# Kernel optimization log

Measured on AMD Instinct MI355X. Metric: run time of the kernel, lower is better.

The kernel has to match this reference:

```python
import jax, jax.numpy as jnp
import numpy as np

SCORE_THRESH = 0.25
NMS_THRESH = 0.45
DETECTIONS = 100   # self.detections
K_CAND = 300       # fixed pre-NMS candidate count (jit-friendly stand-in for torch.where filtering)
STRIDES = (8, 16, 32)


def setup_inputs() -> dict:
    key = jax.random.key(0)
    ks = jax.random.split(key, 5)
    pred_p3 = jax.random.normal(ks[0], (16, 80, 80, 3, 85), jnp.float32)
    pred_p4 = jax.random.normal(ks[1], (16, 40, 40, 3, 85), jnp.float32)
    pred_p5 = jax.random.normal(ks[2], (16, 20, 20, 3, 85), jnp.float32)
    anchors = jnp.array([[[10, 13], [16, 30], [33, 23]],
                         [[30, 61], [62, 45], [59, 119]],
                         [[116, 90], [156, 198], [373, 326]]], jnp.float32)
    image_shapes = jnp.full((16, 2), 640, jnp.int32)  # (h, w) per image
    scale_factors = jax.random.uniform(ks[3], (16,), jnp.float32, 0.5, 1.5)
    return {"pred_p3": pred_p3, "pred_p4": pred_p4, "pred_p5": pred_p5,
            "anchors": anchors, "image_shapes": image_shapes,
            "scale_factors": scale_factors, "max_size": 4096}


def _decode_level(p, stride, anchor_wh):
    # p: [B,H,W,A,5+C] already sigmoided
    B, H, W, A, _ = p.shape
    gx = jnp.arange(W, dtype=p.dtype)
    gy = jnp.arange(H, dtype=p.dtype)
    grid = jnp.stack(jnp.meshgrid(gx, gy, indexing='xy'), axis=-1)  # [H,W,2] = (x,y)
    xy = (2.0 * p[..., :2] - 0.5 + grid[None, :, :, None, :]) * stride
    wh = 4.0 * p[..., 2:4] ** 2 * anchor_wh  # anchor_wh: [A,2]
    box = jnp.concatenate([xy, wh], axis=-1).reshape(B, H * W * A, 4)
    obj = p[..., 4].reshape(B, H * W * A)
    cls = p[..., 5:].reshape(B, H * W * A, -1)
    return box, obj, cls


def _pairwise_iou(b):  # b: [K,4] xyxy
    area = (b[:, 2] - b[:, 0]) * (b[:, 3] - b[:, 1])
    lt = jnp.maximum(b[:, None, :2], b[None, :, :2])
    rb = jnp.minimum(b[:, None, 2:], b[None, :, 2:])
    wh = jnp.clip(rb - lt, 0.0)
    inter = wh[..., 0] * wh[..., 1]
    return inter / (area[:, None] + area[None, :] - inter + 1e-9)


def _nms_image(boxes, scores, labels, im_shape, scale, max_size):
    # boxes [K,4], scores [K] sorted desc, labels [K] int
    w = im_shape[1].astype(boxes.dtype)
    h = im_shape[0].astype(boxes.dtype)
    boxes = jnp.stack([jnp.clip(boxes[:, 0], 0.0, w), jnp.clip(boxes[:, 1], 0.0, h),
                       jnp.clip(boxes[:, 2], 0.0, w), jnp.clip(boxes[:, 3], 0.0, h)], axis=1)
    # class-offset boxes (batched_nms)
    bn = jax.lax.stop_gradient(boxes + (labels.astype(boxes.dtype) * max_size)[:, None])
    iou = _pairwise_iou(bn)
    s_ng = jax.lax.stop_gradient(scores)
    K = boxes.shape[0]
    ar = jnp.arange(K)

    def body(i, keep):
        active = keep[i] & (s_ng[i] > SCORE_THRESH)
        return keep & ~((iou[i] > NMS_THRESH) & (ar > i) & active)

    keep = jax.lax.fori_loop(0, K, body, jnp.ones(K, bool))
    final = jnp.where(keep & (s_ng > SCORE_THRESH), scores, 0.0)
    det_s, det_i = jax.lax.top_k(final, DETECTIONS)
    det_b = boxes[det_i] / scale
    det_l = labels[det_i].astype(boxes.dtype)
    return jnp.concatenate([det_b, det_s[:, None], det_l[:, None]], axis=1)  # [D,6]


def reference(pred_p3, pred_p4, pred_p5, anchors, image_shapes, scale_factors, max_size):
    boxes_l, obj_l, cls_l = [], [], []
    for i, (pred, stride) in enumerate(zip((pred_p3, pred_p4, pred_p5), STRIDES)):
        p = jax.nn.sigmoid(pred)
        b, o, c = _decode_level(p, float(stride), anchors[i])
        boxes_l.append(b); obj_l.append(o); cls_l.append(c)
    boxes = jnp.concatenate(boxes_l, axis=1)   # [B,N,4] cxcywh
    obj = jnp.concatenate(obj_l, axis=1)       # [B,N]
    cls = jnp.concatenate(cls_l, axis=1)       # [B,N,C]
    # cxcywh -> xyxy
    cx, cy, ww, hh = boxes[..., 0], boxes[..., 1], boxes[..., 2], boxes[..., 3]
    boxes = jnp.stack([cx - ww / 2, cy - hh / 2, cx + ww / 2, cy + hh / 2], axis=-1)
    B, N, C = cls.shape
    logits = obj[..., None] * cls              # [B,N,C]
    valid = (obj[..., None] > SCORE_THRESH) & (logits > SCORE_THRESH)
    flat = jnp.where(valid, logits, 0.0).reshape(B, N * C)
    vals, idx = jax.lax.top_k(flat, K_CAND)    # sorted desc per image
    aidx = idx // C
    labels = idx % C
    cand_boxes = jnp.take_along_axis(boxes, aidx[..., None], axis=1)  # [B,K,4]
    out = jax.vmap(_nms_image, in_axes=(0, 0, 0, 0, 0, None))(
        cand_boxes, vals, labels, image_shapes, scale_factors, jnp.float32(max_size))
    return out  # [B, DETECTIONS, 6] = (x1,y1,x2,y2,score,label)
```

## Files before the change

kernel.cpp:

```cpp
#include <hip/hip_runtime.h>
#include <cstdint>
#include <cstddef>

#define BATCH 16
#define NCLS 80
#define NANCH 25200
#define G 48
#define NCHUNK 525
#define TOTCH (BATCH * NCHUNK)
#define CPB 4
#define ABINS 512
#define SBINS 1024
#define ACAP 2048
#define SCAP 2048
#define TILE 64
#define KC 300
#define DET 100
#define SCORE_T 0.25f
#define NMS_T 0.45f

__device__ __forceinline__ float sg(float x) { return 1.0f / (1.0f + expf(-x)); }

__device__ __forceinline__ const float* anchor_base(const float* p3, const float* p4,
                                                    const float* p5, int b, int n) {
    if (n < 19200) return p3 + ((size_t)b * 19200 + n) * 85;
    if (n < 24000) return p4 + ((size_t)b * 4800 + (n - 19200)) * 85;
    return p5 + ((size_t)b * 1200 + (n - 24000)) * 85;
}

struct Chunk { const float4* p; int outbase; };
__device__ __forceinline__ Chunk chunk_of(int g, const float* p3, const float* p4,
                                          const float* p5) {
    Chunk ck;
    int b = g / NCHUNK, ch = g % NCHUNK;
    const float* src; int a0, lvlN, gbase;
    if (ch < 400)      { src = p3; a0 = ch * G;         lvlN = 19200; gbase = 0; }
    else if (ch < 500) { src = p4; a0 = (ch - 400) * G; lvlN = 4800;  gbase = 19200; }
    else               { src = p5; a0 = (ch - 500) * G; lvlN = 1200;  gbase = 24000; }
    ck.p = (const float4*)(src + ((size_t)b * lvlN + a0) * 85);
    ck.outbase = b * NANCH + gbase + a0;
    return ck;
}

__global__ __launch_bounds__(256) void k_max(const float* __restrict__ p3,
                                             const float* __restrict__ p4,
                                             const float* __restrict__ p5,
                                             float* __restrict__ gmax) {
    __shared__ __align__(16) float buf[G * 85];
    __shared__ float pmax[5 * G];
    int tid = threadIdx.x;
    int g0 = blockIdx.x * CPB;
    Chunk cur = chunk_of(g0, p3, p4, p5);
    float4 pre[4];
#pragma unroll
    for (int r = 0; r < 4; r++) {
        int i = tid + r * 256;
        pre[r] = (i < (G * 85 / 4)) ? cur.p[i] : make_float4(0.f, 0.f, 0.f, 0.f);
    }
    for (int it = 0; it < CPB; ++it) {
#pragma unroll
        for (int r = 0; r < 4; r++) {
            int i = tid + r * 256;
            if (i < (G * 85 / 4)) ((float4*)buf)[i] = pre[r];
        }
        Chunk nxt = cur;
        if (it + 1 < CPB) {
            nxt = chunk_of(g0 + it + 1, p3, p4, p5);
#pragma unroll
            for (int r = 0; r < 4; r++) {
                int i = tid + r * 256;
                pre[r] = (i < (G * 85 / 4)) ? nxt.p[i] : make_float4(0.f, 0.f, 0.f, 0.f);
            }
        }
        __syncthreads();
        if (tid < 240) {
            int a = tid % G, part = tid / G;
            const float* base = buf + a * 85 + 5 + part * 16;
            float m = base[0];
#pragma unroll
            for (int k = 1; k < 16; k++) m = fmaxf(m, base[k]);
            pmax[part * G + a] = m;
        }
        __syncthreads();
        if (tid < G) {
            float m = pmax[tid];
#pragma unroll
            for (int p = 1; p < 5; p++) m = fmaxf(m, pmax[p * G + tid]);
            float obj = sg(buf[tid * 85 + 4]);
            float v = 0.0f;
            if (obj > SCORE_T) v = obj * sg(m);
            gmax[cur.outbase + tid] = v;
        }
        __syncthreads();
        cur = nxt;
    }
}

union Ovl {
    struct { float tile[TILE * 85]; } p1;
    struct {
        unsigned long long msk[KC * 5];
        float4 bx[KC];
        int lab[KC];
        float sc2[KC];
        float ar[KC];
        unsigned long long keep[5];
        unsigned int actw[10];
        int wpref[6];
        int order[DET];
        int okept[DET];
    } p2;
};

__global__ __launch_bounds__(1024) void k_img(
    const float* __restrict__ p3, const float* __restrict__ p4, const float* __restrict__ p5,
    const float* __restrict__ anchors, const int* __restrict__ imshapes,
    const float* __restrict__ scalef, const float* __restrict__ gmax,
    float* __restrict__ out) {
    __shared__ unsigned int hist[SBINS];
    __shared__ int alist[ACAP];
    __shared__ __align__(16) Ovl u;
    __shared__ float cs[SCAP];
    __shared__ unsigned int ci[SCAP];
    __shared__ float sv[KC];
    __shared__ unsigned int si[KC];
    __shared__ unsigned int acnt, scnt;
    __shared__ int TaS, TsS;

    int b = blockIdx.x;
    int tid = threadIdx.x;
    const float* gm = gmax + (size_t)b * NANCH;

    hist[tid & (SBINS - 1)] = 0u;
    if (tid == 0) { acnt = 0u; scnt = 0u; TaS = 0; TsS = 0; }
    __syncthreads();
    for (int n = tid; n < NANCH; n += 1024) {
        float v = gm[n];
        if (v > SCORE_T) {
            int bin = (int)((v - SCORE_T) * (ABINS / 0.75f));
            bin = bin < 0 ? 0 : (bin > ABINS - 1 ? ABINS - 1 : bin);
            atomicAdd(&hist[bin], 1u);
        }
    }
    __syncthreads();
    unsigned int run = 0;
    if (tid < ABINS) run = hist[tid];
    __syncthreads();
    for (int off = 1; off < ABINS; off <<= 1) {
        unsigned int add = (tid < ABINS && tid + off < ABINS) ? hist[tid + off] : 0u;
        __syncthreads();
        if (tid < ABINS) { run += add; hist[tid] = run; }
        __syncthreads();
    }
    if (tid < ABINS && run >= KC && (tid == ABINS - 1 || hist[tid + 1] < KC)) TaS = tid;
    __syncthreads();
    int Ta = TaS;

    for (int n = tid; n < NANCH; n += 1024) {
        float v = gm[n];
        if (v > SCORE_T) {
            int bin = (int)((v - SCORE_T) * (ABINS / 0.75f));
            bin = bin < 0 ? 0 : (bin > ABINS - 1 ? ABINS - 1 : bin);
            if (bin >= Ta) {
                unsigned int pos = atomicAdd(&acnt, 1u);
                if (pos < ACAP) alist[pos] = n;
            }
        }
    }
    __syncthreads();
    int M = (int)(acnt < ACAP ? acnt : ACAP);

    hist[tid] = 0u;
    __syncthreads();
    for (int t0 = 0; t0 < M; t0 += TILE) {
        int tc = min(TILE, M - t0);
        for (int idx = tid; idx < tc * 85; idx += 1024) {
            int a = idx / 85, f = idx - a * 85;
            u.p1.tile[idx] = anchor_base(p3, p4, p5, b, alist[t0 + a])[f];
        }
        __syncthreads();
        for (int idx = tid; idx < tc * 80; idx += 1024) {
            int a = idx / 80, c = idx - a * 80;
            float s = sg(u.p1.tile[a * 85 + 4]) * sg(u.p1.tile[a * 85 + 5 + c]);
            if (s > SCORE_T) {
                int bin = (int)((s - SCORE_T) * (SBINS / 0.75f));
                bin = bin < 0 ? 0 : (bin > SBINS - 1 ? SBINS - 1 : bin);
                atomicAdd(&hist[bin], 1u);
            }
        }
        __syncthreads();
    }
    run = hist[tid];
    __syncthreads();
    for (int off = 1; off < SBINS; off <<= 1) {
        unsigned int add = (tid + off < SBINS) ? hist[tid + off] : 0u;
        __syncthreads();
        run += add;
        hist[tid] = run;
        __syncthreads();
    }
    if (run >= KC && (tid == SBINS - 1 || hist[tid + 1] < KC)) TsS = tid;
    __syncthreads();
    int Ts = TsS;

    for (int t0 = 0; t0 < M; t0 += TILE) {
        int tc = min(TILE, M - t0);
        for (int idx = tid; idx < tc * 85; idx += 1024) {
            int a = idx / 85, f = idx - a * 85;
            u.p1.tile[idx] = anchor_base(p3, p4, p5, b, alist[t0 + a])[f];
        }
        __syncthreads();
        for (int idx = tid; idx < tc * 80; idx += 1024) {
            int a = idx / 80, c = idx - a * 80;
            float s = sg(u.p1.tile[a * 85 + 4]) * sg(u.p1.tile[a * 85 + 5 + c]);
            if (s > SCORE_T) {
                int bin = (int)((s - SCORE_T) * (SBINS / 0.75f));
                bin = bin < 0 ? 0 : (bin > SBINS - 1 ? SBINS - 1 : bin);
                if (bin >= Ts) {
                    unsigned int pos = atomicAdd(&scnt, 1u);
                    if (pos < SCAP) {
                        cs[pos] = s;
                        ci[pos] = (unsigned int)(alist[t0 + a] * NCLS + c);
                    }
                }
            }
        }
        __syncthreads();
    }
    int nc = (int)(scnt < SCAP ? scnt : SCAP);

    if (tid < KC) { sv[tid] = 0.f; si[tid] = 0xffffffffu; }
    __syncthreads();
    for (int i = tid; i < nc; i += 1024) {
        float s = cs[i];
        unsigned int ii = ci[i];
        int r = 0;
        for (int j = 0; j < nc; j++) {
            float sj = cs[j];
            unsigned int ij = ci[j];
            if (sj > s || (sj == s && ij < ii)) r++;
        }
        if (r < KC) { sv[r] = s; si[r] = ii; }
    }
    __syncthreads();
    int valid = nc < KC ? nc : KC;

    if (tid < KC) {
        int i = tid;
        if (i < valid) {
            unsigned int fi = si[i];
            int n = (int)(fi / NCLS), c = (int)(fi % NCLS);
            int lvl = (n < 19200) ? 0 : (n < 24000 ? 1 : 2);
            const int offl[3] = {0, 19200, 24000};
            const int Wl[3] = {80, 40, 20};
            const int cntl[3] = {19200, 4800, 1200};
            const float strl[3] = {8.f, 16.f, 32.f};
            const float* pp = lvl == 0 ? p3 : (lvl == 1 ? p4 : p5);
            int nl = n - offl[lvl];
            int a = nl % 3, cell = nl / 3;
            int gx = cell % Wl[lvl], gy = cell / Wl[lvl];
            const float* pb = pp + ((size_t)b * cntl[lvl] + nl) * 85;
            float s0 = sg(pb[0]), s1 = sg(pb[1]), s2 = sg(pb[2]), s3 = sg(pb[3]);
            float stride = strl[lvl];
            float aw = anchors[(lvl * 3 + a) * 2 + 0];
            float ah = anchors[(lvl * 3 + a) * 2 + 1];
            float cx = (2.0f * s0 - 0.5f + (float)gx) * stride;
            float cy = (2.0f * s1 - 0.5f + (float)gy) * stride;
            float bw = 4.0f * s2 * s2 * aw;
            float bh = 4.0f * s3 * s3 * ah;
            float hf = (float)imshapes[b * 2 + 0];
            float wf = (float)imshapes[b * 2 + 1];
            float x1 = cx - bw / 2.0f, y1 = cy - bh / 2.0f;
            float x2 = cx + bw / 2.0f, y2 = cy + bh / 2.0f;
            x1 = fminf(fmaxf(x1, 0.f), wf);
            y1 = fminf(fmaxf(y1, 0.f), hf);
            x2 = fminf(fmaxf(x2, 0.f), wf);
            y2 = fminf(fmaxf(y2, 0.f), hf);
            u.p2.bx[i] = make_float4(x1, y1, x2, y2);
            u.p2.lab[i] = c;
            u.p2.sc2[i] = sv[i];
            u.p2.ar[i] = (x2 - x1) * (y2 - y1);
        } else {
            u.p2.bx[i] = make_float4(0, 0, 0, 0);
            u.p2.lab[i] = -1 - i;
            u.p2.sc2[i] = 0.f;
            u.p2.ar[i] = 0.f;
        }
    }
    __syncthreads();

    if (tid < 10) u.p2.actw[tid] = 0u;
    for (int t = tid; t < KC * 5; t += 1024) {
        int i = t / 5, w = t % 5;
        float4 bi = u.p2.bx[i];
        int li = u.p2.lab[i];
        float ai = u.p2.ar[i];
        unsigned long long m = 0ull;
        for (int tb = 0; tb < 64; tb++) {
            int j = w * 64 + tb;
            if (j < KC && j > i && u.p2.lab[j] == li) {
                float4 bj = u.p2.bx[j];
                float ltx = fmaxf(bi.x, bj.x), lty = fmaxf(bi.y, bj.y);
                float rbx = fminf(bi.z, bj.z), rby = fminf(bi.w, bj.w);
                float iw = fmaxf(rbx - ltx, 0.f), ih = fmaxf(rby - lty, 0.f);
                float inter = iw * ih;
                float iou = inter / (ai + u.p2.ar[j] - inter + 1e-9f);
                if (iou > NMS_T) m |= (1ull << tb);
            }
        }
        u.p2.msk[t] = m;
    }
    __syncthreads();

    for (int i = tid; i < KC; i += 1024) {
        unsigned long long nz = u.p2.msk[i * 5] | u.p2.msk[i * 5 + 1] | u.p2.msk[i * 5 + 2] |
                                u.p2.msk[i * 5 + 3] | u.p2.msk[i * 5 + 4];
        if (nz) atomicOr(&u.p2.actw[i >> 5], 1u << (i & 31));
    }
    __syncthreads();
    if (tid == 0) {
        u.p2.keep[0] = u.p2.keep[1] = u.p2.keep[2] = u.p2.keep[3] = u.p2.keep[4] = ~0ull;
        for (int w = 0; w < 10; w++) {
            unsigned int mw = u.p2.actw[w];
            while (mw) {
                int bpos = __ffs(mw) - 1;
                mw &= mw - 1;
                int i = w * 32 + bpos;
                if ((u.p2.keep[i >> 6] >> (i & 63)) & 1ull) {
#pragma unroll
                    for (int r = 0; r < 5; r++) u.p2.keep[r] &= ~u.p2.msk[i * 5 + r];
                }
            }
        }
        int s = 0;
        for (int w = 0; w < 5; w++) {
            unsigned long long kw = u.p2.keep[w];
            if (w == 4) kw &= (1ull << 44) - 1ull;
            u.p2.wpref[w] = s;
            s += (int)__popcll(kw);
        }
        u.p2.wpref[5] = s;
    }
    __syncthreads();

    if (tid < KC) {
        int w = tid >> 6, bp = tid & 63;
        unsigned long long kw = u.p2.keep[w];
        bool kept = (kw >> bp) & 1ull;
        int r = u.p2.wpref[w] + (int)__popcll(kw & ((1ull << bp) - 1ull));
        if (kept) {
            if (r < DET) { u.p2.order[r] = tid; u.p2.okept[r] = 1; }
        } else {
            int nr = u.p2.wpref[5] + (tid - r);
            if (nr < DET) { u.p2.order[nr] = tid; u.p2.okept[nr] = 0; }
        }
    }
    __syncthreads();

    if (tid < DET) {
        int o = u.p2.order[tid];
        float scale = scalef[b];
        float4 bb = u.p2.bx[o];
        float s = (u.p2.okept[tid] && o < valid) ? u.p2.sc2[o] : 0.f;
        float lb = (o < valid) ? (float)u.p2.lab[o] : 0.f;
        float* po = out + ((size_t)b * DET + tid) * 6;
        po[0] = bb.x / scale;
        po[1] = bb.y / scale;
        po[2] = bb.z / scale;
        po[3] = bb.w / scale;
        po[4] = s;
        po[5] = lb;
    }
}

extern "C" void kernel_launch(void* const* d_in, const int* in_sizes, int n_in,
                              void* d_out, int out_size, void* d_ws, size_t ws_size,
                              hipStream_t stream) {
    const float* p3 = (const float*)d_in[0];
    const float* p4 = (const float*)d_in[1];
    const float* p5 = (const float*)d_in[2];
    const float* anchors = (const float*)d_in[3];
    const int* imshapes = (const int*)d_in[4];
    const float* scalef = (const float*)d_in[5];
    float* out = (float*)d_out;

    float* gmax = (float*)d_ws;

    k_max<<<TOTCH / CPB, 256, 0, stream>>>(p3, p4, p5, gmax);
    k_img<<<BATCH, 1024, 0, stream>>>(p3, p4, p5, anchors, imshapes, scalef, gmax, out);
}
```

Before: 273.6 us.

## Split per-image candidate selection into a multi-block collect kernel with global histograms

Builds the anchor-score histogram with global atomics inside k_max and adds a k_collect kernel that spreads anchor filtering and class-score histogramming over 50 blocks per image. Before, each image used a single 1024-thread block, which serialized this work across only 16 blocks. k_collect writes pre-thresholded class candidates to workspace, and k_img only scans them, picks the final threshold and runs NMS. The cost is a memset, an extra launch, global atomic contention, and a conservative 2*Ta bin cutoff with a fixed 4096 candidate cap that could drop candidates.

After: 282.1 us. +3.1%, slower.

```diff
diff --git a/kernel.cpp b/kernel.cpp
--- a/kernel.cpp
+++ b/kernel.cpp
@@ -11,13 +11,14 @@
 #define CPB 4
 #define ABINS 512
 #define SBINS 1024
-#define ACAP 2048
 #define SCAP 2048
-#define TILE 64
+#define SCAP2 4096
 #define KC 300
 #define DET 100
 #define SCORE_T 0.25f
 #define NMS_T 0.45f
+#define NBLK 50
+#define SPAN 504
 
 __device__ __forceinline__ float sg(float x) { return 1.0f / (1.0f + expf(-x)); }
 
@@ -28,7 +29,7 @@
     return p5 + ((size_t)b * 1200 + (n - 24000)) * 85;
 }
 
-struct Chunk { const float4* p; int outbase; };
+struct Chunk { const float4* p; int outbase; int b; };
 __device__ __forceinline__ Chunk chunk_of(int g, const float* p3, const float* p4,
                                           const float* p5) {
     Chunk ck;
@@ -39,13 +40,15 @@
     else               { src = p5; a0 = (ch - 500) * G; lvlN = 1200;  gbase = 24000; }
     ck.p = (const float4*)(src + ((size_t)b * lvlN + a0) * 85);
     ck.outbase = b * NANCH + gbase + a0;
+    ck.b = b;
     return ck;
 }
 
 __global__ __launch_bounds__(256) void k_max(const float* __restrict__ p3,
                                              const float* __restrict__ p4,
                                              const float* __restrict__ p5,
-                                             float* __restrict__ gmax) {
+                                             float* __restrict__ gmax,
+                                             unsigned int* __restrict__ ahist) {
     __shared__ __align__(16) float buf[G * 85];
     __shared__ float pmax[5 * G];
     int tid = threadIdx.x;
@@ -90,107 +93,121 @@
             float v = 0.0f;
             if (obj > SCORE_T) v = obj * sg(m);
             gmax[cur.outbase + tid] = v;
+            if (v > SCORE_T) {
+                int bin = (int)((v - SCORE_T) * (ABINS / 0.75f));
+                bin = bin < 0 ? 0 : (bin > ABINS - 1 ? ABINS - 1 : bin);
+                atomicAdd(&ahist[cur.b * ABINS + bin], 1u);
+            }
         }
         __syncthreads();
         cur = nxt;
     }
 }
 
-union Ovl {
-    struct { float tile[TILE * 85]; } p1;
-    struct {
-        unsigned long long msk[KC * 5];
-        float4 bx[KC];
-        int lab[KC];
-        float sc2[KC];
-        float ar[KC];
-        unsigned long long keep[5];
-        unsigned int actw[10];
-        int wpref[6];
-        int order[DET];
-        int okept[DET];
-    } p2;
+__global__ __launch_bounds__(512) void k_collect(
+    const float* __restrict__ p3, const float* __restrict__ p4, const float* __restrict__ p5,
+    const float* __restrict__ gmax, const unsigned int* __restrict__ ahist,
+    unsigned int* __restrict__ shist, unsigned int* __restrict__ scnt,
+    float* __restrict__ ss, unsigned int* __restrict__ sidx) {
+    __shared__ unsigned int h[ABINS];
+    __shared__ int TaS;
+    __shared__ int an[SPAN];
+    __shared__ float og[SPAN];
+    __shared__ unsigned int ncand;
+    int tid = threadIdx.x;
+    int b = blockIdx.x / NBLK;
+    int blk = blockIdx.x % NBLK;
+    if (tid == 0) { ncand = 0u; TaS = 0; }
+    h[tid] = ahist[b * ABINS + tid];
+    __syncthreads();
+    unsigned int run = h[tid];
+    __syncthreads();
+    for (int off = 1; off < ABINS; off <<= 1) {
+        unsigned int add = (tid + off < ABINS) ? h[tid + off] : 0u;
+        __syncthreads();
+        run += add;
+        h[tid] = run;
+        __syncthreads();
+    }
+    if (run >= KC && (tid == ABINS - 1 || h[tid + 1] < KC)) TaS = tid;
+    __syncthreads();
+    int Ta = TaS;
+
+    int n0 = blk * SPAN;
+    for (int i = tid; i < SPAN; i += 512) {
+        int n = n0 + i;
+        float v = gmax[(size_t)b * NANCH + n];
+        if (v > SCORE_T) {
+            int bin = (int)((v - SCORE_T) * (ABINS / 0.75f));
+            bin = bin < 0 ? 0 : (bin > ABINS - 1 ? ABINS - 1 : bin);
+            if (bin >= Ta) {
+                unsigned int p = atomicAdd(&ncand, 1u);
+                an[p] = n;
+            }
+        }
+    }
+    __syncthreads();
+    int M = (int)ncand;
+    for (int i = tid; i < M; i += 512) {
+        const float* pb = anchor_base(p3, p4, p5, b, an[i]);
+        og[i] = sg(pb[4]);
+    }
+    __syncthreads();
+    int twoTa = 2 * Ta;
+    for (int idx = tid; idx < M * NCLS; idx += 512) {
+        int a = idx / NCLS, c = idx - a * NCLS;
+        const float* pb = anchor_base(p3, p4, p5, b, an[a]);
+        float s = og[a] * sg(pb[5 + c]);
+        if (s > SCORE_T) {
+            int bin = (int)((s - SCORE_T) * (SBINS / 0.75f));
+            bin = bin < 0 ? 0 : (bin > SBINS - 1 ? SBINS - 1 : bin);
+            if (bin >= twoTa) {
+                atomicAdd(&shist[b * SBINS + bin], 1u);
+                unsigned int p = atomicAdd(&scnt[b], 1u);
+                if (p < SCAP2) {
+                    ss[(size_t)b * SCAP2 + p] = s;
+                    sidx[(size_t)b * SCAP2 + p] = (unsigned int)(an[a] * NCLS + c);
+                }
+            }
+        }
+    }
+}
+
+struct NmsBuf {
+    unsigned long long msk[KC * 5];
+    float4 bx[KC];
+    int lab[KC];
+    float sc2[KC];
+    float ar[KC];
+    unsigned long long keep[5];
+    unsigned int actw[10];
+    int wpref[6];
+    int order[DET];
+    int okept[DET];
 };
 
 __global__ __launch_bounds__(1024) void k_img(
     const float* __restrict__ p3, const float* __restrict__ p4, const float* __restrict__ p5,
     const float* __restrict__ anchors, const int* __restrict__ imshapes,
-    const float* __restrict__ scalef, const float* __restrict__ gmax,
+    const float* __restrict__ scalef,
+    const unsigned int* __restrict__ shist, const unsigned int* __restrict__ scnt_g,
+    const float* __restrict__ ss, const unsigned int* __restrict__ sidx,
     float* __restrict__ out) {
     __shared__ unsigned int hist[SBINS];
-    __shared__ int alist[ACAP];
-    __shared__ __align__(16) Ovl u;
+    __shared__ __align__(16) NmsBuf u;
     __shared__ float cs[SCAP];
     __shared__ unsigned int ci[SCAP];
     __shared__ float sv[KC];
     __shared__ unsigned int si[KC];
-    __shared__ unsigned int acnt, scnt;
-    __shared__ int TaS, TsS;
+    __shared__ unsigned int scnt_s;
+    __shared__ int TsS;
 
     int b = blockIdx.x;
     int tid = threadIdx.x;
-    const float* gm = gmax + (size_t)b * NANCH;
-
-    hist[tid & (SBINS - 1)] = 0u;
-    if (tid == 0) { acnt = 0u; scnt = 0u; TaS = 0; TsS = 0; }
-    __syncthreads();
-    for (int n = tid; n < NANCH; n += 1024) {
-        float v = gm[n];
-        if (v > SCORE_T) {
-            int bin = (int)((v - SCORE_T) * (ABINS / 0.75f));
-            bin = bin < 0 ? 0 : (bin > ABINS - 1 ? ABINS - 1 : bin);
-            atomicAdd(&hist[bin], 1u);
-        }
-    }
-    __syncthreads();
-    unsigned int run = 0;
-    if (tid < ABINS) run = hist[tid];
-    __syncthreads();
-    for (int off = 1; off < ABINS; off <<= 1) {
-        unsigned int add = (tid < ABINS && tid + off < ABINS) ? hist[tid + off] : 0u;
-        __syncthreads();
-        if (tid < ABINS) { run += add; hist[tid] = run; }
-        __syncthreads();
-    }
-    if (tid < ABINS && run >= KC && (tid == ABINS - 1 || hist[tid + 1] < KC)) TaS = tid;
-    __syncthreads();
-    int Ta = TaS;
-
-    for (int n = tid; n < NANCH; n += 1024) {
-        float v = gm[n];
-        if (v > SCORE_T) {
-            int bin = (int)((v - SCORE_T) * (ABINS / 0.75f));
-            bin = bin < 0 ? 0 : (bin > ABINS - 1 ? ABINS - 1 : bin);
-            if (bin >= Ta) {
-                unsigned int pos = atomicAdd(&acnt, 1u);
-                if (pos < ACAP) alist[pos] = n;
-            }
-        }
-    }
-    __syncthreads();
-    int M = (int)(acnt < ACAP ? acnt : ACAP);
-
-    hist[tid] = 0u;
-    __syncthreads();
-    for (int t0 = 0; t0 < M; t0 += TILE) {
-        int tc = min(TILE, M - t0);
-        for (int idx = tid; idx < tc * 85; idx += 1024) {
-            int a = idx / 85, f = idx - a * 85;
-            u.p1.tile[idx] = anchor_base(p3, p4, p5, b, alist[t0 + a])[f];
-        }
-        __syncthreads();
-        for (int idx = tid; idx < tc * 80; idx += 1024) {
-            int a = idx / 80, c = idx - a * 80;
-            float s = sg(u.p1.tile[a * 85 + 4]) * sg(u.p1.tile[a * 85 + 5 + c]);
-            if (s > SCORE_T) {
-                int bin = (int)((s - SCORE_T) * (SBINS / 0.75f));
-                bin = bin < 0 ? 0 : (bin > SBINS - 1 ? SBINS - 1 : bin);
-                atomicAdd(&hist[bin], 1u);
-            }
-        }
-        __syncthreads();
-    }
-    run = hist[tid];
+    if (tid == 0) { scnt_s = 0u; TsS = 0; }
+    hist[tid] = shist[b * SBINS + tid];
+    __syncthreads();
+    unsigned int run = hist[tid];
     __syncthreads();
     for (int off = 1; off < SBINS; off <<= 1) {
         unsigned int add = (tid + off < SBINS) ? hist[tid + off] : 0u;
@@ -203,31 +220,18 @@
     __syncthreads();
     int Ts = TsS;
 
-    for (int t0 = 0; t0 < M; t0 += TILE) {
-        int tc = min(TILE, M - t0);
-        for (int idx = tid; idx < tc * 85; idx += 1024) {
-            int a = idx / 85, f = idx - a * 85;
-            u.p1.tile[idx] = anchor_base(p3, p4, p5, b, alist[t0 + a])[f];
-        }
-        __syncthreads();
-        for (int idx = tid; idx < tc * 80; idx += 1024) {
-            int a = idx / 80, c = idx - a * 80;
-            float s = sg(u.p1.tile[a * 85 + 4]) * sg(u.p1.tile[a * 85 + 5 + c]);
-            if (s > SCORE_T) {
-                int bin = (int)((s - SCORE_T) * (SBINS / 0.75f));
-                bin = bin < 0 ? 0 : (bin > SBINS - 1 ? SBINS - 1 : bin);
-                if (bin >= Ts) {
-                    unsigned int pos = atomicAdd(&scnt, 1u);
-                    if (pos < SCAP) {
-                        cs[pos] = s;
-                        ci[pos] = (unsigned int)(alist[t0 + a] * NCLS + c);
-                    }
-                }
-            }
-        }
-        __syncthreads();
-    }
-    int nc = (int)(scnt < SCAP ? scnt : SCAP);
+    int navail = (int)(scnt_g[b] < SCAP2 ? scnt_g[b] : SCAP2);
+    for (int i = tid; i < navail; i += 1024) {
+        float s = ss[(size_t)b * SCAP2 + i];
+        int bin = (int)((s - SCORE_T) * (SBINS / 0.75f));
+        bin = bin < 0 ? 0 : (bin > SBINS - 1 ? SBINS - 1 : bin);
+        if (bin >= Ts) {
+            unsigned int pos = atomicAdd(&scnt_s, 1u);
+            if (pos < SCAP) { cs[pos] = s; ci[pos] = sidx[(size_t)b * SCAP2 + i]; }
+        }
+    }
+    __syncthreads();
+    int nc = (int)(scnt_s < SCAP ? scnt_s : SCAP);
 
     if (tid < KC) { sv[tid] = 0.f; si[tid] = 0xffffffffu; }
     __syncthreads();
@@ -276,93 +280,93 @@
             y1 = fminf(fmaxf(y1, 0.f), hf);
             x2 = fminf(fmaxf(x2, 0.f), wf);
             y2 = fminf(fmaxf(y2, 0.f), hf);
-            u.p2.bx[i] = make_float4(x1, y1, x2, y2);
-            u.p2.lab[i] = c;
-            u.p2.sc2[i] = sv[i];
-            u.p2.ar[i] = (x2 - x1) * (y2 - y1);
+            u.bx[i] = make_float4(x1, y1, x2, y2);
+            u.lab[i] = c;
+            u.sc2[i] = sv[i];
+            u.ar[i] = (x2 - x1) * (y2 - y1);
         } else {
-            u.p2.bx[i] = make_float4(0, 0, 0, 0);
-            u.p2.lab[i] = -1 - i;
-            u.p2.sc2[i] = 0.f;
-            u.p2.ar[i] = 0.f;
-        }
-    }
-    __syncthreads();
-
-    if (tid < 10) u.p2.actw[tid] = 0u;
+            u.bx[i] = make_float4(0, 0, 0, 0);
+            u.lab[i] = -1 - i;
+            u.sc2[i] = 0.f;
+            u.ar[i] = 0.f;
+        }
+    }
+    __syncthreads();
+
+    if (tid < 10) u.actw[tid] = 0u;
     for (int t = tid; t < KC * 5; t += 1024) {
         int i = t / 5, w = t % 5;
-        float4 bi = u.p2.bx[i];
-        int li = u.p2.lab[i];
-        float ai = u.p2.ar[i];
+        float4 bi = u.bx[i];
+        int li = u.lab[i];
+        float ai = u.ar[i];
         unsigned long long m = 0ull;
         for (int tb = 0; tb < 64; tb++) {
             int j = w * 64 + tb;
-            if (j < KC && j > i && u.p2.lab[j] == li) {
-                float4 bj = u.p2.bx[j];
+            if (j < KC && j > i && u.lab[j] == li) {
+                float4 bj = u.bx[j];
                 float ltx = fmaxf(bi.x, bj.x), lty = fmaxf(bi.y, bj.y);
                 float rbx = fminf(bi.z, bj.z), rby = fminf(bi.w, bj.w);
                 float iw = fmaxf(rbx - ltx, 0.f), ih = fmaxf(rby - lty, 0.f);
                 float inter = iw * ih;
-                float iou = inter / (ai + u.p2.ar[j] - inter + 1e-9f);
+                float iou = inter / (ai + u.ar[j] - inter + 1e-9f);
                 if (iou > NMS_T) m |= (1ull << tb);
             }
         }
-        u.p2.msk[t] = m;
+        u.msk[t] = m;
     }
     __syncthreads();
 
     for (int i = tid; i < KC; i += 1024) {
-        unsigned long long nz = u.p2.msk[i * 5] | u.p2.msk[i * 5 + 1] | u.p2.msk[i * 5 + 2] |
-                                u.p2.msk[i * 5 + 3] | u.p2.msk[i * 5 + 4];
-        if (nz) atomicOr(&u.p2.actw[i >> 5], 1u << (i & 31));
+        unsigned long long nz = u.msk[i * 5] | u.msk[i * 5 + 1] | u.msk[i * 5 + 2] |
+                                u.msk[i * 5 + 3] | u.msk[i * 5 + 4];
+        if (nz) atomicOr(&u.actw[i >> 5], 1u << (i & 31));
     }
     __syncthreads();
     if (tid == 0) {
-        u.p2.keep[0] = u.p2.keep[1] = u.p2.keep[2] = u.p2.keep[3] = u.p2.keep[4] = ~0ull;
+        u.keep[0] = u.keep[1] = u.keep[2] = u.keep[3] = u.keep[4] = ~0ull;
         for (int w = 0; w < 10; w++) {
-            unsigned int mw = u.p2.actw[w];
+            unsigned int mw = u.actw[w];
             while (mw) {
                 int bpos = __ffs(mw) - 1;
                 mw &= mw - 1;
                 int i = w * 32 + bpos;
-                if ((u.p2.keep[i >> 6] >> (i & 63)) & 1ull) {
-#pragma unroll
-                    for (int r = 0; r < 5; r++) u.p2.keep[r] &= ~u.p2.msk[i * 5 + r];
+                if ((u.keep[i >> 6] >> (i & 63)) & 1ull) {
+#pragma unroll
+                    for (int r = 0; r < 5; r++) u.keep[r] &= ~u.msk[i * 5 + r];
                 }
             }
         }
         int s = 0;
         for (int w = 0; w < 5; w++) {
-            unsigned long long kw = u.p2.keep[w];
+            unsigned long long kw = u.keep[w];
             if (w == 4) kw &= (1ull << 44) - 1ull;
-            u.p2.wpref[w] = s;
+            u.wpref[w] = s;
             s += (int)__popcll(kw);
         }
-        u.p2.wpref[5] = s;
+        u.wpref[5] = s;
     }
     __syncthreads();
 
     if (tid < KC) {
         int w = tid >> 6, bp = tid & 63;
-        unsigned long long kw = u.p2.keep[w];
+        unsigned long long kw = u.keep[w];
         bool kept = (kw >> bp) & 1ull;
-        int r = u.p2.wpref[w] + (int)__popcll(kw & ((1ull << bp) - 1ull));
+        int r = u.wpref[w] + (int)__popcll(kw & ((1ull << bp) - 1ull));
         if (kept) {
-            if (r < DET) { u.p2.order[r] = tid; u.p2.okept[r] = 1; }
+            if (r < DET) { u.order[r] = tid; u.okept[r] = 1; }
         } else {
-            int nr = u.p2.wpref[5] + (tid - r);
-            if (nr < DET) { u.p2.order[nr] = tid; u.p2.okept[nr] = 0; }
+            int nr = u.wpref[5] + (tid - r);
+            if (nr < DET) { u.order[nr] = tid; u.okept[nr] = 0; }
         }
     }
     __syncthreads();
 
     if (tid < DET) {
-        int o = u.p2.order[tid];
+        int o = u.order[tid];
         float scale = scalef[b];
-        float4 bb = u.p2.bx[o];
-        float s = (u.p2.okept[tid] && o < valid) ? u.p2.sc2[o] : 0.f;
-        float lb = (o < valid) ? (float)u.p2.lab[o] : 0.f;
+        float4 bb = u.bx[o];
+        float s = (u.okept[tid] && o < valid) ? u.sc2[o] : 0.f;
+        float lb = (o < valid) ? (float)u.lab[o] : 0.f;
         float* po = out + ((size_t)b * DET + tid) * 6;
         po[0] = bb.x / scale;
         po[1] = bb.y / scale;
@@ -384,8 +388,18 @@
     const float* scalef = (const float*)d_in[5];
     float* out = (float*)d_out;
 
-    float* gmax = (float*)d_ws;
-
-    k_max<<<TOTCH / CPB, 256, 0, stream>>>(p3, p4, p5, gmax);
-    k_img<<<BATCH, 1024, 0, stream>>>(p3, p4, p5, anchors, imshapes, scalef, gmax, out);
-}
+    char* ws = (char*)d_ws;
+    float* gmax = (float*)ws;
+    unsigned int* ahist = (unsigned int*)(ws + 1612800);
+    unsigned int* shist = (unsigned int*)(ws + 1612800 + 32768);
+    unsigned int* scnt  = (unsigned int*)(ws + 1612800 + 32768 + 65536);
+    float* ss           = (float*)(ws + 1612800 + 32768 + 65536 + 64);
+    unsigned int* sidx  = (unsigned int*)(ws + 1612800 + 32768 + 65536 + 64 + 262144);
+
+    hipMemsetAsync(ws + 1612800, 0, 32768 + 65536 + 64, stream);
+
+    k_max<<<TOTCH / CPB, 256, 0, stream>>>(p3, p4, p5, gmax, ahist);
+    k_collect<<<BATCH * NBLK, 512, 0, stream>>>(p3, p4, p5, gmax, ahist, shist, scnt, ss, sidx);
+    k_img<<<BATCH, 1024, 0, stream>>>(p3, p4, p5, anchors, imshapes, scalef,
+                                      shist, scnt, ss, sidx, out);
+}
```
